# Kernel optimization log

Measured on AMD Instinct MI355X. Metric: run time of the kernel, lower is better.

## Reference

```python
import jax, jax.numpy as jnp
import numpy as np

B, L, D = 2, 2048, 1024
H = 16
HD = D // H            # 64
HALF = HD // 2         # 32
PHASE_SCALE = 1.0
SCALE = HD ** -0.5


def _orthogonal_projection(rng, d, m):
    g = rng.standard_normal((d, m)).astype(np.float32)
    q, r = np.linalg.qr(g)
    s = np.sign(np.diagonal(r))
    s = np.where(s == 0, 1.0, s).astype(np.float32)
    q = q * s[None, :]
    q = q * np.sqrt(d / m)  # preserve_variance=True
    return jnp.asarray(q)


def setup_inputs() -> dict:
    key = jax.random.key(0)
    ks = jax.random.split(key, 6)
    rng = np.random.default_rng(0)
    return {
        "x": jax.random.normal(ks[0], (B, L, D), dtype=jnp.float32),
        "p": jax.random.normal(ks[1], (B, L, D), dtype=jnp.float32),
        "Wqkv": jax.random.normal(ks[2], (D, 3 * D), dtype=jnp.float32) * (D ** -0.5),
        "bqkv": jax.random.normal(ks[3], (3 * D,), dtype=jnp.float32) * 0.02,
        "Wout": jax.random.normal(ks[4], (D, D), dtype=jnp.float32) * (D ** -0.5),
        "bout": jax.random.normal(ks[5], (D,), dtype=jnp.float32) * 0.02,
        "proj": _orthogonal_projection(rng, D, D // 2),
    }


def _rotate_half(t, cos, sin):
    # non-interleaved rotary: split head_dim in halves
    t1, t2 = t[..., :HALF], t[..., HALF:]
    return jnp.concatenate((t1 * cos - t2 * sin, t1 * sin + t2 * cos), axis=-1)


def reference(x, p, Wqkv, bqkv, Wout, bout, proj):
    Bx, Lx = x.shape[0], x.shape[1]
    # QKV projection -> (B, L, 3, H, HD)
    qkv = (x @ Wqkv + bqkv).reshape(Bx, Lx, 3, H, HD)
    q, k, v = qkv[:, :, 0], qkv[:, :, 1], qkv[:, :, 2]
    # collaborative rotary phases from conditioning tokens p
    phases = (p @ proj).reshape(Bx, Lx, H, HALF) * PHASE_SCALE
    cos, sin = jnp.cos(phases), jnp.sin(phases)
    q = _rotate_half(q, cos, sin)
    k = _rotate_half(k, cos, sin)
    # non-causal softmax attention, scale = head_dim^-0.5
    scores = jnp.einsum("blhd,bmhd->bhlm", q, k) * SCALE
    attn = jax.nn.softmax(scores, axis=-1)
    out = jnp.einsum("bhlm,bmhd->blhd", attn, v).reshape(Bx, Lx, D)
    return out @ Wout + bout
```

## Files before the change

### kernel.cpp

```cpp
#include <hip/hip_runtime.h>


typedef __bf16 bf16;
typedef __bf16 bf16x8 __attribute__((ext_vector_type(8)));
typedef __bf16 bf16x4 __attribute__((ext_vector_type(4)));
typedef float f32x4 __attribute__((ext_vector_type(4)));
typedef float f32x16 __attribute__((ext_vector_type(16)));
typedef unsigned int u32;

__device__ __forceinline__ bf16 f2bf(float f) {
  unsigned u = __builtin_bit_cast(unsigned, f);
  u += 0x7FFFu + ((u >> 16) & 1u);
  unsigned short h = (unsigned short)(u >> 16);
  return __builtin_bit_cast(bf16, h);
}

__device__ __forceinline__ void gload_lds16(const bf16* g, bf16* l) {
  __builtin_amdgcn_global_load_lds((const __attribute__((address_space(1))) u32*)(const void*)g,
                                   (__attribute__((address_space(3))) u32*)(void*)l, 16, 0, 0);
}

__device__ __forceinline__ u32 cvtpk_bf16(float lo, float hi) {
  u32 r;
  asm("v_cvt_pk_bf16_f32 %0, %1, %2" : "=v"(r) : "v"(lo), "v"(hi));
  return r;
}
__device__ __forceinline__ void perm32swap(u32& a, u32& b) {
  asm("v_permlane32_swap_b32 %0, %1" : "+v"(a), "+v"(b));
}

#if __has_builtin(__builtin_amdgcn_exp2f)
#define EXP2(x) __builtin_amdgcn_exp2f(x)
#else
#define EXP2(x) exp2f(x)
#endif

#define QSCALE 0.18033688f

__device__ __forceinline__ void xcd_remap(int& bx, int& by) {
  const int nx = gridDim.x;
  const int nwg = nx * gridDim.y;
  const int lin = blockIdx.y * nx + blockIdx.x;
  const int chunk = nwg >> 3;
  const int nid = (lin & 7) * chunk + (lin >> 3);
  bx = nid % nx;
  by = nid / nx;
}

__global__ __launch_bounds__(256) void k_prep(const float* __restrict__ x, bf16* __restrict__ xb,
                                              const float* __restrict__ p, bf16* __restrict__ pb,
                                              const float* __restrict__ W1, bf16* __restrict__ O1,
                                              const float* __restrict__ W2, bf16* __restrict__ O2,
                                              const float* __restrict__ W3, bf16* __restrict__ O3) {
  const int gb = blockIdx.x;
  if (gb < 8192) {
    int i = gb * 256 + threadIdx.x;
    const float* in = x; bf16* out = xb;
    if (i >= 1048576) { in = p; out = pb; i -= 1048576; }
    const float4 v = ((const float4*)in)[i];
    bf16x4 o;
    o[0] = f2bf(v.x); o[1] = f2bf(v.y); o[2] = f2bf(v.z); o[3] = f2bf(v.w);
    *(bf16x4*)(out + (size_t)i * 4) = o;
    return;
  }
  __shared__ float t[64][65];
  const int lin = gb - 8192;
  int bx = lin % 72;
  const int by = lin / 72;
  const float* in; bf16* out; int C;
  if (bx < 48)      { in = W1; out = O1; C = 3072; }
  else if (bx < 56) { in = W2; out = O2; C = 512;  bx -= 48; }
  else              { in = W3; out = O3; C = 1024; bx -= 56; }
  const int R = 1024;
  const int c0 = bx * 64, r0 = by * 64;
  for (int e = threadIdx.x; e < 4096; e += 256) {
    int r = e >> 6, c = e & 63;
    t[r][c] = in[(size_t)(r0 + r) * C + c0 + c];
  }
  __syncthreads();
  for (int e = threadIdx.x; e < 4096; e += 256) {
    int c = e >> 6, r = e & 63;
    out[(size_t)(c0 + c) * R + r0 + r] = f2bf(t[r][c]);
  }
}

__global__ __launch_bounds__(512, 4) void k_gemm128x64(const bf16* __restrict__ A,
                                                       const bf16* __restrict__ Bt,
                                                       const float* __restrict__ bias,
                                                       float* __restrict__ C,
                                                       int M, int N, int K) {
  __shared__ bf16 sA0[8192], sA1[8192];
  __shared__ bf16 sB0[4096], sB1[4096];
  const int tid = threadIdx.x;
  const int lane = tid & 63, w = tid >> 6;
  const int lrow = lane & 15, lgrp = lane >> 4;
  const int wm = (w >> 1) * 32, wn = (w & 1) * 32;
  int bx, by;
  xcd_remap(bx, by);
  const int m0 = bx * 128, n0 = by * 64;
  const int srow = tid >> 3;
  const int swz8 = ((tid & 7) ^ (srow & 7)) * 8;
  const int r7 = lrow & 7;
  const int nkt = K >> 6;

  const bf16* Ab = A  + (size_t)m0 * K;
  const bf16* Bb = Bt + (size_t)n0 * K;

  f32x4 acc[2][2] = {};

#pragma unroll
  for (int c = 0; c < 2; ++c)
    gload_lds16(Ab + (size_t)(c * 64 + srow) * K + swz8, sA0 + c * 4096 + w * 512);
  gload_lds16(Bb + (size_t)srow * K + swz8, sB0 + w * 512);
  __syncthreads();

  for (int kt = 0; kt < nkt; ++kt) {
    const bf16* pA = (kt & 1) ? sA1 : sA0;
    const bf16* pB = (kt & 1) ? sB1 : sB0;
    bf16* nA = (kt & 1) ? sA0 : sA1;
    bf16* nB = (kt & 1) ? sB0 : sB1;
    const size_t knext = (size_t)(kt + 1) * 64;
    const bool more = (kt < nkt - 1);

#pragma unroll
    for (int kk = 0; kk < 2; ++kk) {
      bf16x8 af[2], bfr[2];
#pragma unroll
      for (int mi = 0; mi < 2; ++mi)
        af[mi] = *(const bf16x8*)&pA[(wm + mi * 16 + lrow) * 64 + ((kk * 4 + lgrp) ^ r7) * 8];
#pragma unroll
      for (int ni = 0; ni < 2; ++ni)
        bfr[ni] = *(const bf16x8*)&pB[(wn + ni * 16 + lrow) * 64 + ((kk * 4 + lgrp) ^ r7) * 8];
      if (more) {
        if (kk == 0) {
#pragma unroll
          for (int c = 0; c < 2; ++c)
            gload_lds16(Ab + (size_t)(c * 64 + srow) * K + knext + swz8, nA + c * 4096 + w * 512);
        } else {
          gload_lds16(Bb + (size_t)srow * K + knext + swz8, nB + w * 512);
        }
      }
      __builtin_amdgcn_s_setprio(1);
#pragma unroll
      for (int mi = 0; mi < 2; ++mi)
#pragma unroll
        for (int ni = 0; ni < 2; ++ni)
          acc[mi][ni] = __builtin_amdgcn_mfma_f32_16x16x32_bf16(af[mi], bfr[ni], acc[mi][ni], 0, 0, 0);
      __builtin_amdgcn_s_setprio(0);
    }
    __syncthreads();
  }

#pragma unroll
  for (int mi = 0; mi < 2; ++mi)
#pragma unroll
    for (int ni = 0; ni < 2; ++ni) {
      const int col = n0 + wn + ni * 16 + lrow;
      const float bv = bias ? bias[col] : 0.f;
#pragma unroll
      for (int j = 0; j < 4; ++j) {
        const int row = m0 + wm + mi * 16 + lgrp * 4 + j;
        C[(size_t)row * N + col] = acc[mi][ni][j] + bv;
      }
    }
}

__global__ __launch_bounds__(512, 2) void k_gemm_qkv256(const bf16* __restrict__ A,
                                                        const bf16* __restrict__ Bt,
                                                        const float* __restrict__ bqkv,
                                                        const float* __restrict__ phases,
                                                        bf16* __restrict__ qb,
                                                        bf16* __restrict__ kb,
                                                        bf16* __restrict__ vb) {
  __shared__ bf16 sA0[16384], sA1[16384];
  __shared__ bf16 sB0[16384], sB1[16384];
  const int tid = threadIdx.x;
  const int lane = tid & 63, w = tid >> 6;
  const int lrow = lane & 15, lgrp = lane >> 4;
  const int wm = (w >> 2) * 128;
  const int wn = (w & 3) * 64;
  const int m0 = blockIdx.x * 256, n0 = blockIdx.y * 256;
  const int K = 1024;

  const int srow = tid >> 3;
  const int swz8 = (((tid & 7) ^ (srow & 7))) * 8;
  const int r7 = lrow & 7;

  const bf16* Ab = A  + (size_t)m0 * K;
  const bf16* Bb = Bt + (size_t)n0 * K;

  f32x4 acc[8][4] = {};

#pragma unroll
  for (int g = 0; g < 4; ++g) {
    gload_lds16(Ab + (size_t)(g * 64 + srow) * K + swz8, sA0 + g * 4096 + w * 512);
    gload_lds16(Bb + (size_t)(g * 64 + srow) * K + swz8, sB0 + g * 4096 + w * 512);
  }
  __syncthreads();

  for (int kt = 0; kt < 16; ++kt) {
    const bf16* pA = (kt & 1) ? sA1 : sA0;
    const bf16* pB = (kt & 1) ? sB1 : sB0;
    bf16* nA = (kt & 1) ? sA0 : sA1;
    bf16* nB = (kt & 1) ? sB0 : sB1;
    const size_t knext = (size_t)(kt + 1) * 64;

    bf16x8 bfr[4][2];
#pragma unroll
    for (int ni = 0; ni < 4; ++ni)
#pragma unroll
      for (int kk = 0; kk < 2; ++kk)
        bfr[ni][kk] = *(const bf16x8*)&pB[(wn + ni * 16 + lrow) * 64 + ((kk * 4 + lgrp) ^ r7) * 8];

#pragma unroll
    for (int q = 0; q < 4; ++q) {
      if (kt < 15) {
        gload_lds16(Ab + (size_t)(q * 64 + srow) * K + knext + swz8, nA + q * 4096 + w * 512);
        gload_lds16(Bb + (size_t)(q * 64 + srow) * K + knext + swz8, nB + q * 4096 + w * 512);
      }
      bf16x8 af[2][2];
#pragma unroll
      for (int m2 = 0; m2 < 2; ++m2)
#pragma unroll
        for (int kk = 0; kk < 2; ++kk)
          af[m2][kk] = *(const bf16x8*)&pA[(wm + (q * 2 + m2) * 16 + lrow) * 64 + ((kk * 4 + lgrp) ^ r7) * 8];
      __builtin_amdgcn_s_setprio(1);
#pragma unroll
      for (int m2 = 0; m2 < 2; ++m2)
#pragma unroll
        for (int ni = 0; ni < 4; ++ni)
#pragma unroll
          for (int kk = 0; kk < 2; ++kk)
            acc[q * 2 + m2][ni] =
                __builtin_amdgcn_mfma_f32_16x16x32_bf16(af[m2][kk], bfr[ni][kk], acc[q * 2 + m2][ni], 0, 0, 0);
      __builtin_amdgcn_s_setprio(0);
    }
    __syncthreads();
  }

  const int nw = n0 + wn;
  const int sec = nw >> 10;
  const int hh = (nw & 1023) >> 6;
  const float b0 = bqkv[nw + lrow];
  const float b1 = bqkv[nw + 16 + lrow];
  const float b2 = bqkv[nw + 32 + lrow];
  const float b3 = bqkv[nw + 48 + lrow];

  if (sec == 2) {
#pragma unroll
    for (int mi = 0; mi < 8; ++mi) {
      const int row0 = m0 + wm + mi * 16 + lgrp * 4;
      const int b = row0 >> 11, l0 = row0 & 2047;
#pragma unroll
      for (int ni = 0; ni < 4; ++ni) {
        const int d = ni * 16 + lrow;
        const float bv = (ni == 0) ? b0 : (ni == 1) ? b1 : (ni == 2) ? b2 : b3;
        bf16x4 pv;
#pragma unroll
        for (int j = 0; j < 4; ++j) pv[j] = f2bf(acc[mi][ni][j] + bv);
        *(bf16x4*)&vb[(((size_t)(b * 16 + hh)) * 64 + d) * 2048 + l0] = pv;
      }
    }
  } else {
    bf16* qk = sec ? kb : qb;
    const float qs = sec ? 1.0f : QSCALE;
#pragma unroll
    for (int mi = 0; mi < 8; ++mi) {
#pragma unroll
      for (int j = 0; j < 4; ++j) {
        const int row = m0 + wm + mi * 16 + lgrp * 4 + j;
        const int b = row >> 11, l = row & 2047;
        const float ph1 = phases[(size_t)row * 512 + hh * 32 + lrow];
        const float ph2 = phases[(size_t)row * 512 + hh * 32 + 16 + lrow];
        float s1, c1, s2, c2;
        __sincosf(ph1, &s1, &c1);
        __sincosf(ph2, &s2, &c2);
        const float t0 = acc[mi][0][j] + b0;
        const float t1 = acc[mi][1][j] + b1;
        const float t2 = acc[mi][2][j] + b2;
        const float t3 = acc[mi][3][j] + b3;
        bf16* base = qk + (((size_t)(b * 16 + hh)) * 2048 + l) * 64;
        base[lrow]      = f2bf((t0 * c1 - t2 * s1) * qs);
        base[16 + lrow] = f2bf((t1 * c2 - t3 * s2) * qs);
        base[32 + lrow] = f2bf((t0 * s1 + t2 * c1) * qs);
        base[48 + lrow] = f2bf((t1 * s2 + t3 * c2) * qs);
      }
    }
  }
}

__global__ __launch_bounds__(256, 4) void k_flash_attn8(const bf16* __restrict__ qb,
                                                        const bf16* __restrict__ kb,
                                                        const bf16* __restrict__ vb,
                                                        bf16* __restrict__ attnout) {
  const int tid = threadIdx.x, lane = tid & 63, w = tid >> 6;
  const int ql = lane & 31, hi = lane >> 5;
  const int tsel = w >> 1;
  const int qh = w & 1;
  const int fid = blockIdx.x;
  const int nid = (fid & 7) * 128 + (fid >> 3);
  const int qblk = nid & 31, h = (nid >> 5) & 15, b = nid >> 9;
  const size_t bh = (size_t)b * 16 + h;
  const bf16* Kp = kb + bh * 2048 * 64;
  const bf16* Vp = vb + bh * 64 * 2048;

  __shared__ __align__(16) char smem[32768];
  bf16* sK = (bf16*)smem;
  bf16* sV = (bf16*)(smem + 16384);

  const bf16* Qp = qb + (bh * 2048 + (size_t)qblk * 64 + qh * 32 + ql) * 64;
  bf16x8 qf[4];
#pragma unroll
  for (int c = 0; c < 4; ++c) qf[c] = *(const bf16x8*)(Qp + c * 16 + hi * 8);

  const int srow = tid >> 3;
  const int swz = (tid & 7) ^ (srow & 7);
  const int jv0 = (tsel * 4 + 0 + hi) ^ (ql & 7);
  const int jv1 = (tsel * 4 + 2 + hi) ^ (ql & 7);

  f32x16 o0 = {}, o1 = {};
  float lsum = 0.f;
  u32 pcu[8];
  bf16x8 vfr[4];

#define STAGE(BUF, KV0)                                                                       \
  do {                                                                                        \
    gload_lds16(Kp + (size_t)((KV0) + srow) * 64 + swz * 8,        sK + (BUF) * 4096 + w * 512); \
    gload_lds16(Kp + (size_t)((KV0) + srow + 32) * 64 + swz * 8,   sK + (BUF) * 4096 + 2048 + w * 512); \
    gload_lds16(Vp + (size_t)srow * 2048 + (KV0) + swz * 8,        sV + (BUF) * 4096 + w * 512); \
    gload_lds16(Vp + (size_t)(srow + 32) * 2048 + (KV0) + swz * 8, sV + (BUF) * 4096 + 2048 + w * 512); \
  } while (0)

#define SM_PACK(CUR)                                                                \
  do {                                                                              \
    const bf16* sVc = sV + (CUR) * 4096;                                            \
    _Pragma("unroll")                                                               \
    for (int j2 = 0; j2 < 16; ++j2) {                                               \
      float pv = EXP2(st0[j2]);                                                     \
      st0[j2] = pv; lsum += pv;                                                     \
    }                                                                               \
    {                                                                               \
      u32 a0 = cvtpk_bf16(st0[0], st0[1]),  a1 = cvtpk_bf16(st0[2], st0[3]);        \
      u32 a2 = cvtpk_bf16(st0[4], st0[5]),  a3 = cvtpk_bf16(st0[6], st0[7]);        \
      perm32swap(a0, a2); perm32swap(a1, a3);                                       \
      pcu[0] = a0; pcu[1] = a1; pcu[2] = a2; pcu[3] = a3;                           \
      u32 b0 = cvtpk_bf16(st0[8], st0[9]),  b1 = cvtpk_bf16(st0[10], st0[11]);      \
      u32 b2 = cvtpk_bf16(st0[12], st0[13]), b3 = cvtpk_bf16(st0[14], st0[15]);     \
      perm32swap(b0, b2); perm32swap(b1, b3);                                       \
      pcu[4] = b0; pcu[5] = b1; pcu[6] = b2; pcu[7] = b3;                           \
    }                                                                               \
    vfr[0] = *(const bf16x8*)&sVc[ql * 64 + jv0 * 8];                               \
    vfr[1] = *(const bf16x8*)&sVc[(32 + ql) * 64 + jv0 * 8];                        \
    vfr[2] = *(const bf16x8*)&sVc[ql * 64 + jv1 * 8];                               \
    vfr[3] = *(const bf16x8*)&sVc[(32 + ql) * 64 + jv1 * 8];                        \
  } while (0)

#define PV_PREV()                                                                   \
  do {                                                                              \
    union { u32 u[4]; bf16x8 v; } cA, cB;                                           \
    cA.u[0] = pcu[0]; cA.u[1] = pcu[1]; cA.u[2] = pcu[2]; cA.u[3] = pcu[3];         \
    cB.u[0] = pcu[4]; cB.u[1] = pcu[5]; cB.u[2] = pcu[6]; cB.u[3] = pcu[7];         \
    __builtin_amdgcn_s_setprio(1);                                                  \
    o0 = __builtin_amdgcn_mfma_f32_32x32x16_bf16(vfr[0], cA.v, o0, 0, 0, 0);        \
    o1 = __builtin_amdgcn_mfma_f32_32x32x16_bf16(vfr[1], cA.v, o1, 0, 0, 0);        \
    o0 = __builtin_amdgcn_mfma_f32_32x32x16_bf16(vfr[2], cB.v, o0, 0, 0, 0);        \
    o1 = __builtin_amdgcn_mfma_f32_32x32x16_bf16(vfr[3], cB.v, o1, 0, 0, 0);        \
    __builtin_amdgcn_s_setprio(0);                                                  \
  } while (0)

  STAGE(0, 0);
  __syncthreads();

  {
    const bf16* sKc = sK;
    f32x16 st0 = {};
#pragma unroll
    for (int c = 0; c < 4; ++c) {
      const int j = (c * 2 + hi) ^ (ql & 7);
      bf16x8 kf = *(const bf16x8*)&sKc[(tsel * 32 + ql) * 64 + j * 8];
      __builtin_amdgcn_s_setprio(1);
      st0 = __builtin_amdgcn_mfma_f32_32x32x16_bf16(kf, qf[c], st0, 0, 0, 0);
      __builtin_amdgcn_s_setprio(0);
    }
    STAGE(1, 64);
    SM_PACK(0);
    __syncthreads();
  }

  for (int t = 1; t < 32; ++t) {
    const int cur = t & 1;
    const bf16* sKc = sK + cur * 4096;

    f32x16 st0 = {};
#pragma unroll
    for (int c = 0; c < 4; ++c) {
      const int j = (c * 2 + hi) ^ (ql & 7);
      bf16x8 kf = *(const bf16x8*)&sKc[(tsel * 32 + ql) * 64 + j * 8];
      __builtin_amdgcn_s_setprio(1);
      st0 = __builtin_amdgcn_mfma_f32_32x32x16_bf16(kf, qf[c], st0, 0, 0, 0);
      __builtin_amdgcn_s_setprio(0);
    }
    PV_PREV();
    if (t < 31) STAGE(cur ^ 1, (t + 1) * 64);
    SM_PACK(cur);
    __syncthreads();
  }

  PV_PREV();

  float* cb = (float*)smem;
  if (w >= 2) {
    const int idx = ((w - 2) * 64 + lane) * 34;
#pragma unroll
    for (int i = 0; i < 16; ++i) cb[idx + i] = o0[i];
#pragma unroll
    for (int i = 0; i < 16; ++i) cb[idx + 16 + i] = o1[i];
    cb[idx + 32] = lsum;
  }
  __syncthreads();
  if (w < 2) {
    const int idx = (w * 64 + lane) * 34;
#pragma unroll
    for (int i = 0; i < 16; ++i) o0[i] += cb[idx + i];
#pragma unroll
    for (int i = 0; i < 16; ++i) o1[i] += cb[idx + 16 + i];
    lsum += cb[idx + 32];
    lsum += __shfl_xor(lsum, 32);

    const float inv = 1.f / lsum;
    const int qrow = qblk * 64 + qh * 32 + ql;
    bf16* outp = attnout + ((size_t)b * 2048 + qrow) * 1024 + h * 64;
#pragma unroll
    for (int j2 = 0; j2 < 4; ++j2) {
      bf16x4 ov;
#pragma unroll
      for (int jj = 0; jj < 4; ++jj) ov[jj] = f2bf(o0[j2 * 4 + jj] * inv);
      *(bf16x4*)(outp + j2 * 8 + hi * 4) = ov;
#pragma unroll
      for (int jj = 0; jj < 4; ++jj) ov[jj] = f2bf(o1[j2 * 4 + jj] * inv);
      *(bf16x4*)(outp + 32 + j2 * 8 + hi * 4) = ov;
    }
  }
#undef STAGE
#undef SM_PACK
#undef PV_PREV
}

extern "C" void kernel_launch(void* const* d_in, const int* in_sizes, int n_in,
                              void* d_out, int out_size, void* d_ws, size_t ws_size,
                              hipStream_t stream) {
  (void)in_sizes; (void)n_in; (void)out_size; (void)ws_size;
  const float* x    = (const float*)d_in[0];
  const float* p    = (const float*)d_in[1];
  const float* Wqkv = (const float*)d_in[2];
  const float* bqkv = (const float*)d_in[3];
  const float* Wout = (const float*)d_in[4];
  const float* bout = (const float*)d_in[5];
  const float* proj = (const float*)d_in[6];
  float* out = (float*)d_out;

  char* ws = (char*)d_ws;
  size_t off = 0;
  bf16* xb     = (bf16*)(ws + off); off += (size_t)4096 * 1024 * 2;
  bf16* pb     = (bf16*)(ws + off); off += (size_t)4096 * 1024 * 2;
  bf16* WqkvT  = (bf16*)(ws + off); off += (size_t)3072 * 1024 * 2;
  bf16* projT  = (bf16*)(ws + off); off += (size_t)512  * 1024 * 2;
  bf16* WoutT  = (bf16*)(ws + off); off += (size_t)1024 * 1024 * 2;
  float* phases= (float*)(ws + off); off += (size_t)4096 * 512 * 4;
  bf16* qb     = (bf16*)(ws + off); off += (size_t)4096 * 1024 * 2;
  bf16* kb     = (bf16*)(ws + off); off += (size_t)4096 * 1024 * 2;
  bf16* vb     = (bf16*)(ws + off); off += (size_t)4096 * 1024 * 2;
  bf16* attnb  = (bf16*)(ws + off); off += (size_t)4096 * 1024 * 2;

  k_prep<<<9344, 256, 0, stream>>>(x, xb, p, pb, Wqkv, WqkvT, proj, projT, Wout, WoutT);

  k_gemm128x64<<<dim3(32, 8), 512, 0, stream>>>(pb, projT, nullptr, phases, 4096, 512, 1024);
  k_gemm_qkv256<<<dim3(16, 12), 512, 0, stream>>>(xb, WqkvT, bqkv, phases, qb, kb, vb);

  k_flash_attn8<<<1024, 256, 0, stream>>>(qb, kb, vb, attnb);

  k_gemm128x64<<<dim3(32, 16), 512, 0, stream>>>(attnb, WoutT, bout, out, 4096, 1024, 1024);
}
```

Before: 129.9 us.

## Triple-buffer K tiles and prefetch K fragments into registers in flash attention

```diff
diff --git a/kernel.cpp b/kernel.cpp
--- a/kernel.cpp
+++ b/kernel.cpp
@@ -289,7 +289,7 @@
   }
 }
 
-__global__ __launch_bounds__(256, 4) void k_flash_attn8(const bf16* __restrict__ qb,
+__global__ __launch_bounds__(256, 4) void k_flash_attn9(const bf16* __restrict__ qb,
                                                         const bf16* __restrict__ kb,
                                                         const bf16* __restrict__ vb,
                                                         bf16* __restrict__ attnout) {
@@ -304,9 +304,9 @@
   const bf16* Kp = kb + bh * 2048 * 64;
   const bf16* Vp = vb + bh * 64 * 2048;
 
-  __shared__ __align__(16) char smem[32768];
-  bf16* sK = (bf16*)smem;
-  bf16* sV = (bf16*)(smem + 16384);
+  __shared__ __align__(16) char smem[40960];
+  bf16* sKb[3] = { (bf16*)smem, (bf16*)(smem + 8192), (bf16*)(smem + 16384) };
+  bf16* sVb[2] = { (bf16*)(smem + 24576), (bf16*)(smem + 32768) };
 
   const bf16* Qp = qb + (bh * 2048 + (size_t)qblk * 64 + qh * 32 + ql) * 64;
   bf16x8 qf[4];
@@ -315,25 +315,39 @@
 
   const int srow = tid >> 3;
   const int swz = (tid & 7) ^ (srow & 7);
+  const int jk0 = (0 * 2 + hi) ^ (ql & 7), jk1 = (1 * 2 + hi) ^ (ql & 7);
+  const int jk2 = (2 * 2 + hi) ^ (ql & 7), jk3 = (3 * 2 + hi) ^ (ql & 7);
   const int jv0 = (tsel * 4 + 0 + hi) ^ (ql & 7);
   const int jv1 = (tsel * 4 + 2 + hi) ^ (ql & 7);
+  const int krow = (tsel * 32 + ql) * 64;
 
   f32x16 o0 = {}, o1 = {};
   float lsum = 0.f;
   u32 pcu[8];
   bf16x8 vfr[4];
-
-#define STAGE(BUF, KV0)                                                                       \
-  do {                                                                                        \
-    gload_lds16(Kp + (size_t)((KV0) + srow) * 64 + swz * 8,        sK + (BUF) * 4096 + w * 512); \
-    gload_lds16(Kp + (size_t)((KV0) + srow + 32) * 64 + swz * 8,   sK + (BUF) * 4096 + 2048 + w * 512); \
-    gload_lds16(Vp + (size_t)srow * 2048 + (KV0) + swz * 8,        sV + (BUF) * 4096 + w * 512); \
-    gload_lds16(Vp + (size_t)(srow + 32) * 2048 + (KV0) + swz * 8, sV + (BUF) * 4096 + 2048 + w * 512); \
+  bf16x8 kfn[4];
+
+#define STAGE_K(PTR, KV0)                                                                    \
+  do {                                                                                       \
+    gload_lds16(Kp + (size_t)((KV0) + srow) * 64 + swz * 8,      (PTR) + w * 512);           \
+    gload_lds16(Kp + (size_t)((KV0) + srow + 32) * 64 + swz * 8, (PTR) + 2048 + w * 512);    \
   } while (0)
-
-#define SM_PACK(CUR)                                                                \
+#define STAGE_V(PTR, KV0)                                                                    \
+  do {                                                                                       \
+    gload_lds16(Vp + (size_t)srow * 2048 + (KV0) + swz * 8,        (PTR) + w * 512);         \
+    gload_lds16(Vp + (size_t)(srow + 32) * 2048 + (KV0) + swz * 8, (PTR) + 2048 + w * 512);  \
+  } while (0)
+
+#define KF_PREFETCH(PTR)                                       \
+  do {                                                         \
+    kfn[0] = *(const bf16x8*)&(PTR)[krow + jk0 * 8];           \
+    kfn[1] = *(const bf16x8*)&(PTR)[krow + jk1 * 8];           \
+    kfn[2] = *(const bf16x8*)&(PTR)[krow + jk2 * 8];           \
+    kfn[3] = *(const bf16x8*)&(PTR)[krow + jk3 * 8];           \
+  } while (0)
+
+#define SM_PACK(VPTR)                                                               \
   do {                                                                              \
-    const bf16* sVc = sV + (CUR) * 4096;                                            \
     _Pragma("unroll")                                                               \
     for (int j2 = 0; j2 < 16; ++j2) {                                               \
       float pv = EXP2(st0[j2]);                                                     \
@@ -349,10 +363,10 @@
       perm32swap(b0, b2); perm32swap(b1, b3);                                       \
       pcu[4] = b0; pcu[5] = b1; pcu[6] = b2; pcu[7] = b3;                           \
     }                                                                               \
-    vfr[0] = *(const bf16x8*)&sVc[ql * 64 + jv0 * 8];                               \
-    vfr[1] = *(const bf16x8*)&sVc[(32 + ql) * 64 + jv0 * 8];                        \
-    vfr[2] = *(const bf16x8*)&sVc[ql * 64 + jv1 * 8];                               \
-    vfr[3] = *(const bf16x8*)&sVc[(32 + ql) * 64 + jv1 * 8];                        \
+    vfr[0] = *(const bf16x8*)&(VPTR)[ql * 64 + jv0 * 8];                            \
+    vfr[1] = *(const bf16x8*)&(VPTR)[(32 + ql) * 64 + jv0 * 8];                     \
+    vfr[2] = *(const bf16x8*)&(VPTR)[ql * 64 + jv1 * 8];                            \
+    vfr[3] = *(const bf16x8*)&(VPTR)[(32 + ql) * 64 + jv1 * 8];                     \
   } while (0)
 
 #define PV_PREV()                                                                   \
@@ -368,42 +382,53 @@
     __builtin_amdgcn_s_setprio(0);                                                  \
   } while (0)
 
-  STAGE(0, 0);
+  bf16 *ka = sKb[0], *kbuf = sKb[1], *kc = sKb[2];
+  bf16 *va = sVb[0], *vbuf = sVb[1];
+
+  STAGE_K(ka, 0);
+  STAGE_K(kbuf, 64);
+  STAGE_V(va, 0);
   __syncthreads();
 
   {
-    const bf16* sKc = sK;
     f32x16 st0 = {};
-#pragma unroll
-    for (int c = 0; c < 4; ++c) {
-      const int j = (c * 2 + hi) ^ (ql & 7);
-      bf16x8 kf = *(const bf16x8*)&sKc[(tsel * 32 + ql) * 64 + j * 8];
-      __builtin_amdgcn_s_setprio(1);
-      st0 = __builtin_amdgcn_mfma_f32_32x32x16_bf16(kf, qf[c], st0, 0, 0, 0);
-      __builtin_amdgcn_s_setprio(0);
-    }
-    STAGE(1, 64);
-    SM_PACK(0);
+    bf16x8 kf0 = *(const bf16x8*)&ka[krow + jk0 * 8];
+    bf16x8 kf1 = *(const bf16x8*)&ka[krow + jk1 * 8];
+    bf16x8 kf2 = *(const bf16x8*)&ka[krow + jk2 * 8];
+    bf16x8 kf3 = *(const bf16x8*)&ka[krow + jk3 * 8];
+    __builtin_amdgcn_s_setprio(1);
+    st0 = __builtin_amdgcn_mfma_f32_32x32x16_bf16(kf0, qf[0], st0, 0, 0, 0);
+    st0 = __builtin_amdgcn_mfma_f32_32x32x16_bf16(kf1, qf[1], st0, 0, 0, 0);
+    st0 = __builtin_amdgcn_mfma_f32_32x32x16_bf16(kf2, qf[2], st0, 0, 0, 0);
+    st0 = __builtin_amdgcn_mfma_f32_32x32x16_bf16(kf3, qf[3], st0, 0, 0, 0);
+    __builtin_amdgcn_s_setprio(0);
+    KF_PREFETCH(kbuf);
+    STAGE_K(kc, 128);
+    STAGE_V(vbuf, 64);
+    SM_PACK(va);
     __syncthreads();
+    bf16* tmp = ka; ka = kbuf; kbuf = kc; kc = tmp;
+    bf16* tv = va; va = vbuf; vbuf = tv;
   }
 
   for (int t = 1; t < 32; ++t) {
-    const int cur = t & 1;
-    const bf16* sKc = sK + cur * 4096;
-
     f32x16 st0 = {};
-#pragma unroll
-    for (int c = 0; c < 4; ++c) {
-      const int j = (c * 2 + hi) ^ (ql & 7);
-      bf16x8 kf = *(const bf16x8*)&sKc[(tsel * 32 + ql) * 64 + j * 8];
-      __builtin_amdgcn_s_setprio(1);
-      st0 = __builtin_amdgcn_mfma_f32_32x32x16_bf16(kf, qf[c], st0, 0, 0, 0);
-      __builtin_amdgcn_s_setprio(0);
-    }
+    __builtin_amdgcn_s_setprio(1);
+    st0 = __builtin_amdgcn_mfma_f32_32x32x16_bf16(kfn[0], qf[0], st0, 0, 0, 0);
+    st0 = __builtin_amdgcn_mfma_f32_32x32x16_bf16(kfn[1], qf[1], st0, 0, 0, 0);
+    st0 = __builtin_amdgcn_mfma_f32_32x32x16_bf16(kfn[2], qf[2], st0, 0, 0, 0);
+    st0 = __builtin_amdgcn_mfma_f32_32x32x16_bf16(kfn[3], qf[3], st0, 0, 0, 0);
+    __builtin_amdgcn_s_setprio(0);
     PV_PREV();
-    if (t < 31) STAGE(cur ^ 1, (t + 1) * 64);
-    SM_PACK(cur);
+    if (t < 31) {
+      KF_PREFETCH(kbuf);
+      if (t < 30) STAGE_K(kc, (t + 2) * 64);
+      STAGE_V(vbuf, (t + 1) * 64);
+    }
+    SM_PACK(va);
     __syncthreads();
+    bf16* tmp = ka; ka = kbuf; kbuf = kc; kc = tmp;
+    bf16* tv = va; va = vbuf; vbuf = tv;
   }
 
   PV_PREV();
@@ -441,7 +466,9 @@
       *(bf16x4*)(outp + 32 + j2 * 8 + hi * 4) = ov;
     }
   }
-#undef STAGE
+#undef STAGE_K
+#undef STAGE_V
+#undef KF_PREFETCH
 #undef SM_PACK
 #undef PV_PREV
 }
@@ -477,7 +504,7 @@
   k_gemm128x64<<<dim3(32, 8), 512, 0, stream>>>(pb, projT, nullptr, phases, 4096, 512, 1024);
   k_gemm_qkv256<<<dim3(16, 12), 512, 0, stream>>>(xb, WqkvT, bqkv, phases, qb, kb, vb);
 
-  k_flash_attn8<<<1024, 256, 0, stream>>>(qb, kb, vb, attnb);
+  k_flash_attn9<<<1024, 256, 0, stream>>>(qb, kb, vb, attnb);
 
   k_gemm128x64<<<dim3(32, 16), 512, 0, stream>>>(attnb, WoutT, bout, out, 4096, 1024, 1024);
 }
```

Measured after the change: 129.6 us. About the same (-0.2%).
